# Kernel tuning notes

Measured on AMD Instinct MI355X. Metric: run time of the kernel, lower is better.

Reference implementation:

```python
import jax, jax.numpy as jnp
import numpy as np


def dct2_mat(N):
    # Orthonormal DCT-II matrix M[k, n]; scipy dct(norm='ortho') == M @ x,
    # and since M is orthogonal, idct(norm='ortho') == M.T @ x.
    n = jnp.arange(N, dtype=jnp.float32)
    k = jnp.arange(N, dtype=jnp.float32)[:, None]
    M = jnp.cos(jnp.pi * (n + 0.5) * k / N)
    scale = jnp.where(k == 0, jnp.sqrt(1.0 / N), jnp.sqrt(2.0 / N))
    return (M * scale).astype(jnp.float32)


def setup_inputs() -> dict:
    key = jax.random.key(0)
    x = jax.random.normal(key, (8, 32, 64, 64, 64), dtype=jnp.float32)
    return {"x": x}


def reference(x):
    # Faithful to original: DCT is applied along B, D, H (axes 0,1,2 of the
    # permuted [B,D,H,W,C] tensor), crop/pad acts on D,H,W, then IDCT along B,D,H.
    OUT = (32, 32, 32)
    TR = (32, 32, 32)
    B, C, D, H, W = x.shape
    CB, CD, CH = dct2_mat(B), dct2_mat(D), dct2_mat(H)

    # forward DCT-II (ortho) along B, D, H as batched matmuls
    y = jnp.einsum('kb,bcdhw->kcdhw', CB, x)
    y = jnp.einsum('kd,bcdhw->bckhw', CD, y)
    y = jnp.einsum('kh,bcdhw->bcdkw', CH, y)

    # spectral crop along D, H, W, then zero-pad up to output_size
    y = y[:, :, :TR[0], :TR[1], :TR[2]]
    y = jnp.pad(y, ((0, 0), (0, 0),
                    (0, OUT[0] - TR[0]),
                    (0, OUT[1] - TR[1]),
                    (0, OUT[2] - TR[2])))

    # inverse DCT (ortho) = transpose of the (orthogonal) DCT matrix
    Bi, Di, Hi = y.shape[0], y.shape[2], y.shape[3]
    z = jnp.einsum('kn,kcdhw->ncdhw', dct2_mat(Bi), y)
    z = jnp.einsum('kn,bckhw->bcnhw', dct2_mat(Di), z)
    z = jnp.einsum('kn,bcdkw->bcdnw', dct2_mat(Hi), z)
    return z
```

## Files before the change

kernel.cpp:

```cpp
#include <hip/hip_runtime.h>
#include <math.h>


__global__ void build_A_kernel(float* __restrict__ A, float* __restrict__ At) {
  int idx = blockIdx.x * blockDim.x + threadIdx.x;
  if (idx >= 32 * 64) return;
  int n = idx >> 6;
  int h = idx & 63;
  const float s32a = sqrtf(1.0f / 32.0f), s32b = sqrtf(2.0f / 32.0f);
  const float s64a = sqrtf(1.0f / 64.0f), s64b = sqrtf(2.0f / 64.0f);
  float s = 0.0f;
  for (int k = 0; k < 32; ++k) {
    float c32 = cosf((float)M_PI * ((float)n + 0.5f) * (float)k / 32.0f) * ((k == 0) ? s32a : s32b);
    float c64 = cosf((float)M_PI * ((float)h + 0.5f) * (float)k / 64.0f) * ((k == 0) ? s64a : s64b);
    s = fmaf(c32, c64, s);
  }
  A[n * 64 + h] = s;
  At[h * 32 + n] = s;
}

__global__ __launch_bounds__(1024, 4) void spectral_kernel(
    const float* __restrict__ x, const float* __restrict__ A,
    const float* __restrict__ At, float* __restrict__ out) {
  __shared__ float V[32][32][32];

  const int tid = threadIdx.x;
  const int bc = blockIdx.x;
  const int wv = tid >> 6;
  const int dloc = tid >> 5;
  const int w = tid & 31;
  const int nhq = (tid >> 4) & 3;
  const int w16 = tid & 15;
  const int ndg = wv & 7;
  const int jg = wv >> 3;

  const float* xb = x + (size_t)bc * 262144;

  float acc[4][4][2];
  #pragma unroll
  for (int i = 0; i < 4; ++i)
    #pragma unroll
    for (int j = 0; j < 4; ++j) {
      acc[i][j][0] = 0.f;
      acc[i][j][1] = 0.f;
    }

  #pragma unroll 1
  for (int cc = 0; cc < 2; ++cc) {
    const int d = cc * 32 + dloc;
    const float* xcol = xb + (size_t)d * 4096 + w;

    float p[32];
    #pragma unroll
    for (int nh = 0; nh < 32; ++nh) p[nh] = 0.f;

    float cur[16], nxt[16];
    #pragma unroll
    for (int i = 0; i < 16; ++i) cur[i] = xcol[i * 64];

    #pragma unroll 1
    for (int hc = 0; hc < 4; ++hc) {
      if (hc < 3) {
        #pragma unroll
        for (int i = 0; i < 16; ++i) nxt[i] = xcol[(hc * 16 + 16 + i) * 64];
      }
      #pragma unroll
      for (int nh = 0; nh < 32; ++nh) {
        const float* Ar = A + nh * 64 + hc * 16;
        float s = p[nh];
        #pragma unroll
        for (int i = 0; i < 16; ++i) s = fmaf(Ar[i], cur[i], s);
        p[nh] = s;
      }
      #pragma unroll
      for (int i = 0; i < 16; ++i) cur[i] = nxt[i];
    }

    #pragma unroll
    for (int nh = 0; nh < 32; ++nh) V[dloc][nh][w] = p[nh];
    __syncthreads();

    #pragma unroll 1
    for (int dd = 0; dd < 32; ++dd) {
      const int dg = cc * 32 + dd;
      const float* Acol = At + dg * 32 + ndg * 4;
      const float a0 = Acol[0], a1 = Acol[1], a2 = Acol[2], a3 = Acol[3];
      #pragma unroll
      for (int j = 0; j < 4; ++j) {
        const int nh = (jg * 4 + j) * 4 + nhq;
        const float2 v = *(const float2*)&V[dd][nh][w16 * 2];
        acc[0][j][0] = fmaf(a0, v.x, acc[0][j][0]);
        acc[0][j][1] = fmaf(a0, v.y, acc[0][j][1]);
        acc[1][j][0] = fmaf(a1, v.x, acc[1][j][0]);
        acc[1][j][1] = fmaf(a1, v.y, acc[1][j][1]);
        acc[2][j][0] = fmaf(a2, v.x, acc[2][j][0]);
        acc[2][j][1] = fmaf(a2, v.y, acc[2][j][1]);
        acc[3][j][0] = fmaf(a3, v.x, acc[3][j][0]);
        acc[3][j][1] = fmaf(a3, v.y, acc[3][j][1]);
      }
    }
    __syncthreads();
  }

  float* ob = out + (size_t)bc * 32768;
  #pragma unroll
  for (int i = 0; i < 4; ++i) {
    const int nd = ndg * 4 + i;
    #pragma unroll
    for (int j = 0; j < 4; ++j) {
      const int nh = (jg * 4 + j) * 4 + nhq;
      float2 v;
      v.x = acc[i][j][0];
      v.y = acc[i][j][1];
      *(float2*)(ob + nd * 1024 + nh * 32 + w16 * 2) = v;
    }
  }
}

extern "C" void kernel_launch(void* const* d_in, const int* in_sizes, int n_in,
                              void* d_out, int out_size, void* d_ws, size_t ws_size,
                              hipStream_t stream) {
  const float* x = (const float*)d_in[0];
  float* A = (float*)d_ws;
  float* At = A + 2048;
  build_A_kernel<<<32, 64, 0, stream>>>(A, At);
  spectral_kernel<<<256, 1024, 0, stream>>>(x, A, At, (float*)d_out);
}
```

Measured before the change: 368.3 us.

## Bake DCT crop matrix as compile-time constants and drop the build kernel

Computes the combined 32x64 crop matrix at compile time with constexpr cosine and sqrt, so stage-one weights become immediate constants folded into the FMAs and the separate build kernel launch disappears. The second stage reads a pre-packed float4 table from device constant memory instead of four scalar loads. The stage-one loop is fully unrolled with explicit double-buffered loads, the shared tile is padded to 33 columns, and the dd loop is unrolled by 8. Risks include register pressure and code bloat from the inlined literals, and the padding may misalign the float2 shared loads.

```diff
diff --git a/kernel.cpp b/kernel.cpp
--- a/kernel.cpp
+++ b/kernel.cpp
@@ -1,28 +1,89 @@
 #include <hip/hip_runtime.h>
-#include <math.h>
 
 
-__global__ void build_A_kernel(float* __restrict__ A, float* __restrict__ At) {
-  int idx = blockIdx.x * blockDim.x + threadIdx.x;
-  if (idx >= 32 * 64) return;
-  int n = idx >> 6;
-  int h = idx & 63;
-  const float s32a = sqrtf(1.0f / 32.0f), s32b = sqrtf(2.0f / 32.0f);
-  const float s64a = sqrtf(1.0f / 64.0f), s64b = sqrtf(2.0f / 64.0f);
-  float s = 0.0f;
-  for (int k = 0; k < 32; ++k) {
-    float c32 = cosf((float)M_PI * ((float)n + 0.5f) * (float)k / 32.0f) * ((k == 0) ? s32a : s32b);
-    float c64 = cosf((float)M_PI * ((float)h + 0.5f) * (float)k / 64.0f) * ((k == 0) ? s64a : s64b);
-    s = fmaf(c32, c64, s);
+constexpr double kPI = 3.14159265358979323846;
+
+constexpr double cos_poly(double x) {
+  double r = 1.0;
+  for (int k = 15; k >= 1; --k) r = 1.0 - r * x * x / ((2.0 * k) * (2.0 * k - 1.0));
+  return r;
+}
+constexpr double csqrt(double v) {
+  double r = (v > 1.0) ? v : 1.0;
+  for (int i = 0; i < 64; ++i) r = 0.5 * (r + v / r);
+  return r;
+}
+
+struct C64T  { double c[128]; };
+struct C128T { double c[256]; };
+constexpr C64T make_c64() {
+  C64T t{};
+  for (int m = 0; m < 128; ++m) {
+    int mm = (m > 64) ? m - 128 : m;
+    t.c[m] = cos_poly(kPI * (double)mm / 64.0);
   }
-  A[n * 64 + h] = s;
-  At[h * 32 + n] = s;
+  return t;
+}
+constexpr C128T make_c128() {
+  C128T t{};
+  for (int m = 0; m < 256; ++m) {
+    int mm = (m > 128) ? m - 256 : m;
+    t.c[m] = cos_poly(kPI * (double)mm / 128.0);
+  }
+  return t;
+}
+constexpr C64T  C64_  = make_c64();
+constexpr C128T C128_ = make_c128();
+
+struct ATabH { float a[16 * 64]; };
+constexpr ATabH make_A_half(int n0) {
+  ATabH t{};
+  const double s32a = csqrt(1.0 / 32.0), s32b = csqrt(2.0 / 32.0);
+  const double s64a = csqrt(1.0 / 64.0), s64b = csqrt(2.0 / 64.0);
+  for (int ni = 0; ni < 16; ++ni)
+    for (int h = 0; h < 64; ++h) {
+      const int n = n0 + ni;
+      double s = 0.0;
+      for (int k = 0; k < 32; ++k) {
+        double sc = ((k == 0) ? s32a : s32b) * ((k == 0) ? s64a : s64b);
+        s += sc * C64_.c[((2 * n + 1) * k) % 128] * C128_.c[((2 * h + 1) * k) % 256];
+      }
+      t.a[ni * 64 + h] = (float)s;
+    }
+  return t;
+}
+constexpr ATabH A_LO = make_A_half(0);
+constexpr ATabH A_HI = make_A_half(16);
+
+__host__ __device__ constexpr float Aval(int n, int h) {
+  return (n < 16) ? A_LO.a[n * 64 + h] : A_HI.a[(n - 16) * 64 + h];
+}
+
+struct AT2Tab { float a[8 * 64 * 4]; };
+constexpr AT2Tab make_AT2() {
+  AT2Tab t{};
+  for (int ndg = 0; ndg < 8; ++ndg)
+    for (int dg = 0; dg < 64; ++dg)
+      for (int i = 0; i < 4; ++i)
+        t.a[(ndg * 64 + dg) * 4 + i] = Aval(ndg * 4 + i, dg);
+  return t;
+}
+__device__ const AT2Tab AT2_DEV = make_AT2();
+
+template <int HB>
+__device__ __forceinline__ void s1_group(float (&p)[32], const float (&xr)[16]) {
+#pragma unroll
+  for (int nh = 0; nh < 32; ++nh) {
+    float s = p[nh];
+#pragma unroll
+    for (int i = 0; i < 16; ++i) s = fmaf(Aval(nh, HB + i), xr[i], s);
+    p[nh] = s;
+  }
 }
 
 __global__ __launch_bounds__(1024, 4) void spectral_kernel(
-    const float* __restrict__ x, const float* __restrict__ A,
-    const float* __restrict__ At, float* __restrict__ out) {
-  __shared__ float V[32][32][32];
+    const float* __restrict__ x, float* __restrict__ out) {
+  __shared__ float V[32][32][33];
 
   const int tid = threadIdx.x;
   const int bc = blockIdx.x;
@@ -37,76 +98,67 @@
   const float* xb = x + (size_t)bc * 262144;
 
   float acc[4][4][2];
-  #pragma unroll
+#pragma unroll
   for (int i = 0; i < 4; ++i)
-    #pragma unroll
+#pragma unroll
     for (int j = 0; j < 4; ++j) {
       acc[i][j][0] = 0.f;
       acc[i][j][1] = 0.f;
     }
 
-  #pragma unroll 1
+#pragma unroll 1
   for (int cc = 0; cc < 2; ++cc) {
     const int d = cc * 32 + dloc;
     const float* xcol = xb + (size_t)d * 4096 + w;
 
     float p[32];
-    #pragma unroll
+#pragma unroll
     for (int nh = 0; nh < 32; ++nh) p[nh] = 0.f;
 
-    float cur[16], nxt[16];
-    #pragma unroll
-    for (int i = 0; i < 16; ++i) cur[i] = xcol[i * 64];
+    float xa[16], xc[16];
+#pragma unroll
+    for (int i = 0; i < 16; ++i) xa[i] = xcol[i * 64];
+#pragma unroll
+    for (int i = 0; i < 16; ++i) xc[i] = xcol[(16 + i) * 64];
+    s1_group<0>(p, xa);
+#pragma unroll
+    for (int i = 0; i < 16; ++i) xa[i] = xcol[(32 + i) * 64];
+    s1_group<16>(p, xc);
+#pragma unroll
+    for (int i = 0; i < 16; ++i) xc[i] = xcol[(48 + i) * 64];
+    s1_group<32>(p, xa);
+    s1_group<48>(p, xc);
 
-    #pragma unroll 1
-    for (int hc = 0; hc < 4; ++hc) {
-      if (hc < 3) {
-        #pragma unroll
-        for (int i = 0; i < 16; ++i) nxt[i] = xcol[(hc * 16 + 16 + i) * 64];
-      }
-      #pragma unroll
-      for (int nh = 0; nh < 32; ++nh) {
-        const float* Ar = A + nh * 64 + hc * 16;
-        float s = p[nh];
-        #pragma unroll
-        for (int i = 0; i < 16; ++i) s = fmaf(Ar[i], cur[i], s);
-        p[nh] = s;
-      }
-      #pragma unroll
-      for (int i = 0; i < 16; ++i) cur[i] = nxt[i];
-    }
-
-    #pragma unroll
+#pragma unroll
     for (int nh = 0; nh < 32; ++nh) V[dloc][nh][w] = p[nh];
     __syncthreads();
 
-    #pragma unroll 1
+    const float4* at4 = (const float4*)(AT2_DEV.a) + ndg * 64 + cc * 32;
+#pragma unroll 8
     for (int dd = 0; dd < 32; ++dd) {
-      const int dg = cc * 32 + dd;
-      const float* Acol = At + dg * 32 + ndg * 4;
-      const float a0 = Acol[0], a1 = Acol[1], a2 = Acol[2], a3 = Acol[3];
-      #pragma unroll
+      const float4 a4 = at4[dd];
+#pragma unroll
       for (int j = 0; j < 4; ++j) {
         const int nh = (jg * 4 + j) * 4 + nhq;
         const float2 v = *(const float2*)&V[dd][nh][w16 * 2];
-        acc[0][j][0] = fmaf(a0, v.x, acc[0][j][0]);
-        acc[0][j][1] = fmaf(a0, v.y, acc[0][j][1]);
-        acc[1][j][0] = fmaf(a1, v.x, acc[1][j][0]);
-        acc[1][j][1] = fmaf(a1, v.y, acc[1][j][1]);
-        acc[2][j][0] = fmaf(a2, v.x, acc[2][j][0]);
-        acc[2][j][1] = fmaf(a2, v.y, acc[2][j][1]);
-        acc[3][j][0] = fmaf(a3, v.x, acc[3][j][0]);
-        acc[3][j][1] = fmaf(a3, v.y, acc[3][j][1]);
+        acc[0][j][0] = fmaf(a4.x, v.x, acc[0][j][0]);
+        acc[0][j][1] = fmaf(a4.x, v.y, acc[0][j][1]);
+        acc[1][j][0] = fmaf(a4.y, v.x, acc[1][j][0]);
+        acc[1][j][1] = fmaf(a4.y, v.y, acc[1][j][1]);
+        acc[2][j][0] = fmaf(a4.z, v.x, acc[2][j][0]);
+        acc[2][j][1] = fmaf(a4.z, v.y, acc[2][j][1]);
+        acc[3][j][0] = fmaf(a4.w, v.x, acc[3][j][0]);
+        acc[3][j][1] = fmaf(a4.w, v.y, acc[3][j][1]);
       }
     }
     __syncthreads();
   }
 
   float* ob = out + (size_t)bc * 32768;
-  #pragma unroll
+#pragma unroll
   for (int i = 0; i < 4; ++i) {
     const int nd = ndg * 4 + i;
-    #pragma unroll
+#pragma unroll
     for (int j = 0; j < 4; ++j) {
       const int nh = (jg * 4 + j) * 4 + nhq;
       float2 v;
@@ -121,8 +173,5 @@
                               void* d_out, int out_size, void* d_ws, size_t ws_size,
                               hipStream_t stream) {
   const float* x = (const float*)d_in[0];
-  float* A = (float*)d_ws;
-  float* At = A + 2048;
-  build_A_kernel<<<32, 64, 0, stream>>>(A, At);
-  spectral_kernel<<<256, 1024, 0, stream>>>(x, A, At, (float*)d_out);
+  spectral_kernel<<<256, 1024, 0, stream>>>(x, (float*)d_out);
 }
```

Measured after the change: 344.9 us. -6.4%, faster.
